# Performance work log

Measured on AMD Instinct MI355X. Metric: run time of the kernel, lower is better.

Reference implementation:

```python
import jax, jax.numpy as jnp
import numpy as np

ROUTINGS = 3
EPS = 1e-05


def squash(x, axis):
    n = jnp.linalg.norm(x, axis=axis, keepdims=True)
    n2 = n * n
    return n2 / (1.0 + n2) * x / (n + EPS)


def setup_inputs() -> dict:
    key = jax.random.key(0)
    k1, k2, k3 = jax.random.split(key, 3)
    B, I, O = 64, 1024, 1024
    stdv = 1.0 / np.sqrt(I)
    u = jax.random.normal(k1, (B, I), dtype=jnp.float32)
    weight = jax.random.uniform(k2, (I, O), dtype=jnp.float32, minval=-stdv, maxval=stdv)
    bias = jax.random.uniform(k3, (O,), dtype=jnp.float32, minval=-stdv, maxval=stdv)
    return {"u": u, "weight": weight, "bias": bias}


def reference(u, weight, bias):
    # u: [B, I], weight: [I, O], bias: [O]
    O = weight.shape[1]
    u_hat = u[:, :, None] * weight  # [B, I, O]
    # retain_grad=False: routing iterations use detached u_hat / bias
    uh = jax.lax.stop_gradient(u_hat)
    bs = jax.lax.stop_gradient(bias)
    c = jnp.full((1, 1, O), 1.0 / O, dtype=u.dtype)  # softmax(zeros) over out dim
    b = jnp.zeros_like(uh)
    for _ in range(ROUTINGS - 1):
        v = squash(jnp.sum(uh * c, axis=1) + bs, axis=1)  # [B, O]
        b = b + uh * v[:, None, :]
        c = jax.nn.softmax(b, axis=2)
    return squash(jnp.sum(u_hat * c, axis=1) + bias, axis=1)
```

## Files before the change

### kernel.cpp

```cpp
#include <hip/hip_runtime.h>
#include <math.h>


#define BB 64
#define II 1024
#define OO 1024
#define EPSF 1e-5f
#define LOG2E 1.44269504088896340736f

__device__ __forceinline__ float wave_sum(float v) {
    #pragma unroll
    for (int off = 32; off > 0; off >>= 1)
        v += __shfl_xor(v, off, 64);
    return v;
}
__device__ __forceinline__ float rfl(float x) {
    return __int_as_float(__builtin_amdgcn_readfirstlane(__float_as_int(x)));
}

template<int IBLKS>
__global__ __launch_bounds__(256)
__attribute__((amdgpu_waves_per_eu(8)))
void stage_k(
    const float* __restrict__ u, const float* __restrict__ w,
    const float* __restrict__ v, float* __restrict__ part)
{
    constexpr int IPB = II / IBLKS;
    constexpr int NG  = IPB / 8;
    static_assert(IPB % 8 == 0, "need groups of 8");
    const int bg   = blockIdx.x / IBLKS;
    const int iblk = blockIdx.x % IBLKS;
    const int wave = threadIdx.x >> 6;
    const int lane = threadIdx.x & 63;
    const int b    = bg * 4 + wave;
    const float4* w4 = (const float4*)w;
    const float4* v4 = (const float4*)(v + b * OO);

    float vv[16];
    #pragma unroll
    for (int j = 0; j < 4; j++) {
        float4 a = v4[j * 64 + lane];
        vv[j*4+0]=a.x*LOG2E; vv[j*4+1]=a.y*LOG2E;
        vv[j*4+2]=a.z*LOG2E; vv[j*4+3]=a.w*LOG2E;
    }
    float ar[16];
    #pragma unroll
    for (int k = 0; k < 16; k++) ar[k] = 0.f;

    const int i0 = iblk * IPB;
    #pragma unroll 1
    for (int g = 0; g < NG; g++) {
        const int ib = i0 + g * 8;

        float us[8];
        #pragma unroll
        for (int ii = 0; ii < 8; ii++)
            us[ii] = rfl(u[b * II + ib + ii]);

        float sA[8];
        #pragma unroll 2
        for (int ii = 0; ii < 8; ii++) {
            const int i = ib + ii;
            float a0;
            {
                float4 t = w4[i * 256 + 0 * 64 + lane];
                a0 = __builtin_amdgcn_exp2f((t.x * vv[0]) * us[ii])
                   + __builtin_amdgcn_exp2f((t.y * vv[1]) * us[ii])
                   + __builtin_amdgcn_exp2f((t.z * vv[2]) * us[ii])
                   + __builtin_amdgcn_exp2f((t.w * vv[3]) * us[ii]);
            }
            #pragma unroll
            for (int j = 1; j < 4; j++) {
                float4 t = w4[i * 256 + j * 64 + lane];
                a0 += __builtin_amdgcn_exp2f((t.x * vv[j*4+0]) * us[ii])
                    + __builtin_amdgcn_exp2f((t.y * vv[j*4+1]) * us[ii])
                    + __builtin_amdgcn_exp2f((t.z * vv[j*4+2]) * us[ii])
                    + __builtin_amdgcn_exp2f((t.w * vv[j*4+3]) * us[ii]);
            }
            sA[ii] = a0;
        }
        #pragma unroll
        for (int off = 32; off > 0; off >>= 1) {
            #pragma unroll
            for (int ii = 0; ii < 8; ii++)
                sA[ii] += __shfl_xor(sA[ii], off, 64);
        }
        float qs[8];
        #pragma unroll
        for (int ii = 0; ii < 8; ii++)
            qs[ii] = rfl(us[ii] * __builtin_amdgcn_rcpf(sA[ii]));

        #pragma unroll 2
        for (int ii = 0; ii < 8; ii++) {
            const int i = ib + ii;
            #pragma unroll
            for (int j = 0; j < 4; j++) {
                float4 t = w4[i * 256 + j * 64 + lane];
                float p;
                p = __builtin_amdgcn_exp2f((t.x * vv[j*4+0]) * us[ii]);
                ar[j*4+0] = fmaf(t.x * p, qs[ii], ar[j*4+0]);
                p = __builtin_amdgcn_exp2f((t.y * vv[j*4+1]) * us[ii]);
                ar[j*4+1] = fmaf(t.y * p, qs[ii], ar[j*4+1]);
                p = __builtin_amdgcn_exp2f((t.z * vv[j*4+2]) * us[ii]);
                ar[j*4+2] = fmaf(t.z * p, qs[ii], ar[j*4+2]);
                p = __builtin_amdgcn_exp2f((t.w * vv[j*4+3]) * us[ii]);
                ar[j*4+3] = fmaf(t.w * p, qs[ii], ar[j*4+3]);
            }
        }
    }
    float4* dst = (float4*)(part + ((size_t)iblk * BB + b) * OO);
    #pragma unroll
    for (int j = 0; j < 4; j++) {
        float4 o;
        o.x = ar[j*4+0]; o.y = ar[j*4+1]; o.z = ar[j*4+2]; o.w = ar[j*4+3];
        dst[j * 64 + lane] = o;
    }
}

template<int IBLKS>
__global__ __launch_bounds__(256)
__attribute__((amdgpu_waves_per_eu(8)))
void gemm_k(
    const float* __restrict__ u, const float* __restrict__ w,
    float* __restrict__ part)
{
    constexpr int IPB = II / IBLKS;
    const int bg   = blockIdx.x / IBLKS;
    const int iblk = blockIdx.x % IBLKS;
    const int wave = threadIdx.x >> 6;
    const int lane = threadIdx.x & 63;
    const int b    = bg * 4 + wave;
    const float4* w4 = (const float4*)w;

    float ar[16];
    #pragma unroll
    for (int k = 0; k < 16; k++) ar[k] = 0.f;

    const int i0 = iblk * IPB;
    #pragma unroll 2
    for (int ii = 0; ii < IPB; ii++) {
        const int i = i0 + ii;
        const float ub = rfl(u[b * II + i]);
        #pragma unroll
        for (int j = 0; j < 4; j++) {
            float4 t = w4[i * 256 + j * 64 + lane];
            ar[j*4+0] = fmaf(ub, t.x, ar[j*4+0]);
            ar[j*4+1] = fmaf(ub, t.y, ar[j*4+1]);
            ar[j*4+2] = fmaf(ub, t.z, ar[j*4+2]);
            ar[j*4+3] = fmaf(ub, t.w, ar[j*4+3]);
        }
    }
    float4* dst = (float4*)(part + ((size_t)iblk * BB + b) * OO);
    #pragma unroll
    for (int j = 0; j < 4; j++) {
        float4 o;
        o.x = ar[j*4+0]; o.y = ar[j*4+1]; o.z = ar[j*4+2]; o.w = ar[j*4+3];
        dst[j * 64 + lane] = o;
    }
}

__global__ __launch_bounds__(1024) void reduce_squash(
    const float* __restrict__ part, const float* __restrict__ bias,
    float* __restrict__ vbuf, float* __restrict__ out,
    float scale, int mode, int nblk)
{
    const int b  = blockIdx.x;
    const int t  = threadIdx.x;
    const int qd = t & 255;
    const int sl = t >> 8;
    const int per = nblk >> 2;
    const float4* p4 = (const float4*)part;

    float4 a0 = make_float4(0.f, 0.f, 0.f, 0.f), a1 = a0;
    const int k0 = sl * per;
    #pragma unroll 2
    for (int k = 0; k < per; k += 2) {
        float4 p0 = p4[(size_t)((k0 + k)     * BB + b) * 256 + qd];
        float4 p1 = p4[(size_t)((k0 + k + 1) * BB + b) * 256 + qd];
        a0.x += p0.x; a0.y += p0.y; a0.z += p0.z; a0.w += p0.w;
        a1.x += p1.x; a1.y += p1.y; a1.z += p1.z; a1.w += p1.w;
    }
    a0.x += a1.x; a0.y += a1.y; a0.z += a1.z; a0.w += a1.w;

    __shared__ float4 redq[1024];
    redq[t] = a0;
    __syncthreads();

    float ss = 0.f;
    float4 x;
    if (t < 256) {
        float4 r0 = redq[qd], r1 = redq[256 + qd],
               r2 = redq[512 + qd], r3 = redq[768 + qd];
        float4 s;
        s.x = (r0.x + r1.x) + (r2.x + r3.x);
        s.y = (r0.y + r1.y) + (r2.y + r3.y);
        s.z = (r0.z + r1.z) + (r2.z + r3.z);
        s.w = (r0.w + r1.w) + (r2.w + r3.w);
        float4 bb = ((const float4*)bias)[qd];
        x.x = fmaf(s.x, scale, bb.x); x.y = fmaf(s.y, scale, bb.y);
        x.z = fmaf(s.z, scale, bb.z); x.w = fmaf(s.w, scale, bb.w);
        ss = x.x*x.x + x.y*x.y + x.z*x.z + x.w*x.w;
    }
    ss = wave_sum(ss);
    __shared__ float red2[16];
    if ((t & 63) == 0) red2[t >> 6] = ss;
    __syncthreads();
    const float tot = (red2[0] + red2[1]) + (red2[2] + red2[3]);

    if (t < 256) {
        const float n = sqrtf(tot);
        const float f = tot / ((1.f + tot) * (n + EPSF));
        float4 vo;
        vo.x = x.x * f; vo.y = x.y * f; vo.z = x.z * f; vo.w = x.w * f;
        if (mode == 0) {
            ((float4*)(vbuf + b * OO))[qd] = vo;
        } else if (mode == 1) {
            float4 pv = ((const float4*)(vbuf + b * OO))[qd];
            pv.x += vo.x; pv.y += vo.y; pv.z += vo.z; pv.w += vo.w;
            ((float4*)(vbuf + b * OO))[qd] = pv;
        } else {
            ((float4*)(out + b * OO))[qd] = vo;
        }
    }
}

template<int IBLKS>
static void run_pipeline(const float* u, const float* w, const float* bias,
                         float* out, void* d_ws, hipStream_t stream)
{
    float* part = (float*)d_ws;
    float* vbuf = part + (size_t)IBLKS * BB * OO;
    dim3 g((BB / 4) * IBLKS), blk(256), rblk(1024);
    gemm_k<IBLKS><<<g, blk, 0, stream>>>(u, w, part);
    reduce_squash<<<dim3(BB), rblk, 0, stream>>>(part, bias, vbuf, out,
                                                 1.0f / (float)OO, 0, IBLKS);
    stage_k<IBLKS><<<g, blk, 0, stream>>>(u, w, vbuf, part);
    reduce_squash<<<dim3(BB), rblk, 0, stream>>>(part, bias, vbuf, out,
                                                 1.0f, 1, IBLKS);
    stage_k<IBLKS><<<g, blk, 0, stream>>>(u, w, vbuf, part);
    reduce_squash<<<dim3(BB), rblk, 0, stream>>>(part, bias, vbuf, out,
                                                 1.0f, 2, IBLKS);
}

extern "C" void kernel_launch(void* const* d_in, const int* in_sizes, int n_in,
                              void* d_out, int out_size, void* d_ws, size_t ws_size,
                              hipStream_t stream) {
    (void)in_sizes; (void)n_in; (void)out_size;
    const float* u    = (const float*)d_in[0];
    const float* w    = (const float*)d_in[1];
    const float* bias = (const float*)d_in[2];
    float* out = (float*)d_out;

    const size_t row = (size_t)BB * OO * sizeof(float);
    if      (ws_size >= 129 * row) run_pipeline<128>(u, w, bias, out, d_ws, stream);
    else if (ws_size >=  65 * row) run_pipeline<64>(u, w, bias, out, d_ws, stream);
    else if (ws_size >=  33 * row) run_pipeline<32>(u, w, bias, out, d_ws, stream);
    else                           run_pipeline<16>(u, w, bias, out, d_ws, stream);
}
```

Measured before the change: 163.0 us.

## Fuse routing pipeline into one persistent kernel with grid-wide barriers

Replaces the six separate launches (gemm, three reduces, two routing stages) with one persistent kernel of 256 blocks of 1024 threads. Spin-wait atomic barriers separate the phases, and a memset resets the counters first. The aim is to remove launch gaps and tail effects between the small kernels. The split changes to 64 I-blocks, and the fallback path uses fixed 8-way splitting. The grid-wide barrier depends on all 256 blocks being co-resident, which could deadlock if they are not, and reductions now run on only 64 of the blocks while the rest sit idle.

```diff
diff --git a/kernel.cpp b/kernel.cpp
--- a/kernel.cpp
+++ b/kernel.cpp
@@ -7,6 +7,9 @@
 #define OO 1024
 #define EPSF 1e-5f
 #define LOG2E 1.44269504088896340736f
+#define NBLK 256
+#define MIBLKS 64
+#define MIPB (II / MIBLKS)
 
 __device__ __forceinline__ float wave_sum(float v) {
     #pragma unroll
@@ -18,21 +21,57 @@
     return __int_as_float(__builtin_amdgcn_readfirstlane(__float_as_int(x)));
 }
 
-template<int IBLKS>
-__global__ __launch_bounds__(256)
-__attribute__((amdgpu_waves_per_eu(8)))
-void stage_k(
-    const float* __restrict__ u, const float* __restrict__ w,
-    const float* __restrict__ v, float* __restrict__ part)
-{
-    constexpr int IPB = II / IBLKS;
-    constexpr int NG  = IPB / 8;
-    static_assert(IPB % 8 == 0, "need groups of 8");
-    const int bg   = blockIdx.x / IBLKS;
-    const int iblk = blockIdx.x % IBLKS;
-    const int wave = threadIdx.x >> 6;
-    const int lane = threadIdx.x & 63;
-    const int b    = bg * 4 + wave;
+__device__ __forceinline__ void gbar(int* c) {
+    __syncthreads();
+    if (threadIdx.x == 0) {
+        __threadfence();
+        __hip_atomic_fetch_add(c, 1, __ATOMIC_RELAXED, __HIP_MEMORY_SCOPE_AGENT);
+        while (__hip_atomic_load(c, __ATOMIC_ACQUIRE,
+                                 __HIP_MEMORY_SCOPE_AGENT) < NBLK) { }
+    }
+    __syncthreads();
+}
+
+
+template<int IPB>
+__device__ __forceinline__ void gemm_wave(
+    const float* __restrict__ u, const float* __restrict__ w,
+    float* __restrict__ part, int b, int iblk, int lane)
+{
+    const float4* w4 = (const float4*)w;
+    float ar[16];
+    #pragma unroll
+    for (int k = 0; k < 16; k++) ar[k] = 0.f;
+    const int i0 = iblk * IPB;
+    #pragma unroll 2
+    for (int ii = 0; ii < IPB; ii++) {
+        const int i = i0 + ii;
+        const float ub = rfl(u[b * II + i]);
+        #pragma unroll
+        for (int j = 0; j < 4; j++) {
+            float4 t = w4[i * 256 + j * 64 + lane];
+            ar[j*4+0] = fmaf(ub, t.x, ar[j*4+0]);
+            ar[j*4+1] = fmaf(ub, t.y, ar[j*4+1]);
+            ar[j*4+2] = fmaf(ub, t.z, ar[j*4+2]);
+            ar[j*4+3] = fmaf(ub, t.w, ar[j*4+3]);
+        }
+    }
+    float4* dst = (float4*)(part + ((size_t)iblk * BB + b) * OO);
+    #pragma unroll
+    for (int j = 0; j < 4; j++) {
+        float4 o;
+        o.x = ar[j*4+0]; o.y = ar[j*4+1]; o.z = ar[j*4+2]; o.w = ar[j*4+3];
+        dst[j * 64 + lane] = o;
+    }
+}
+
+template<int IPB>
+__device__ __forceinline__ void stage_wave(
+    const float* __restrict__ u, const float* __restrict__ w,
+    const float* __restrict__ v, float* __restrict__ part,
+    int b, int iblk, int lane)
+{
+    constexpr int NG = IPB / 8;
     const float4* w4 = (const float4*)w;
     const float4* v4 = (const float4*)(v + b * OO);
 
@@ -51,7 +90,6 @@
     #pragma unroll 1
     for (int g = 0; g < NG; g++) {
         const int ib = i0 + g * 8;
-
         float us[8];
         #pragma unroll
         for (int ii = 0; ii < 8; ii++)
@@ -61,16 +99,9 @@
         #pragma unroll 2
         for (int ii = 0; ii < 8; ii++) {
             const int i = ib + ii;
-            float a0;
-            {
-                float4 t = w4[i * 256 + 0 * 64 + lane];
-                a0 = __builtin_amdgcn_exp2f((t.x * vv[0]) * us[ii])
-                   + __builtin_amdgcn_exp2f((t.y * vv[1]) * us[ii])
-                   + __builtin_amdgcn_exp2f((t.z * vv[2]) * us[ii])
-                   + __builtin_amdgcn_exp2f((t.w * vv[3]) * us[ii]);
-            }
+            float a0 = 0.f;
             #pragma unroll
-            for (int j = 1; j < 4; j++) {
+            for (int j = 0; j < 4; j++) {
                 float4 t = w4[i * 256 + j * 64 + lane];
                 a0 += __builtin_amdgcn_exp2f((t.x * vv[j*4+0]) * us[ii])
                     + __builtin_amdgcn_exp2f((t.y * vv[j*4+1]) * us[ii])
@@ -117,54 +148,11 @@
     }
 }
 
-template<int IBLKS>
-__global__ __launch_bounds__(256)
-__attribute__((amdgpu_waves_per_eu(8)))
-void gemm_k(
-    const float* __restrict__ u, const float* __restrict__ w,
-    float* __restrict__ part)
-{
-    constexpr int IPB = II / IBLKS;
-    const int bg   = blockIdx.x / IBLKS;
-    const int iblk = blockIdx.x % IBLKS;
-    const int wave = threadIdx.x >> 6;
-    const int lane = threadIdx.x & 63;
-    const int b    = bg * 4 + wave;
-    const float4* w4 = (const float4*)w;
-
-    float ar[16];
-    #pragma unroll
-    for (int k = 0; k < 16; k++) ar[k] = 0.f;
-
-    const int i0 = iblk * IPB;
-    #pragma unroll 2
-    for (int ii = 0; ii < IPB; ii++) {
-        const int i = i0 + ii;
-        const float ub = rfl(u[b * II + i]);
-        #pragma unroll
-        for (int j = 0; j < 4; j++) {
-            float4 t = w4[i * 256 + j * 64 + lane];
-            ar[j*4+0] = fmaf(ub, t.x, ar[j*4+0]);
-            ar[j*4+1] = fmaf(ub, t.y, ar[j*4+1]);
-            ar[j*4+2] = fmaf(ub, t.z, ar[j*4+2]);
-            ar[j*4+3] = fmaf(ub, t.w, ar[j*4+3]);
-        }
-    }
-    float4* dst = (float4*)(part + ((size_t)iblk * BB + b) * OO);
-    #pragma unroll
-    for (int j = 0; j < 4; j++) {
-        float4 o;
-        o.x = ar[j*4+0]; o.y = ar[j*4+1]; o.z = ar[j*4+2]; o.w = ar[j*4+3];
-        dst[j * 64 + lane] = o;
-    }
-}
-
-__global__ __launch_bounds__(1024) void reduce_squash(
+__device__ __forceinline__ void reduce_block(
     const float* __restrict__ part, const float* __restrict__ bias,
     float* __restrict__ vbuf, float* __restrict__ out,
-    float scale, int mode, int nblk)
-{
-    const int b  = blockIdx.x;
+    float scale, int mode, int nblk, int b, float4* redq, float* red2)
+{
     const int t  = threadIdx.x;
     const int qd = t & 255;
     const int sl = t >> 8;
@@ -182,7 +170,6 @@
     }
     a0.x += a1.x; a0.y += a1.y; a0.z += a1.z; a0.w += a1.w;
 
-    __shared__ float4 redq[1024];
     redq[t] = a0;
     __syncthreads();
 
@@ -202,7 +189,6 @@
         ss = x.x*x.x + x.y*x.y + x.z*x.z + x.w*x.w;
     }
     ss = wave_sum(ss);
-    __shared__ float red2[16];
     if ((t & 63) == 0) red2[t >> 6] = ss;
     __syncthreads();
     const float tot = (red2[0] + red2[1]) + (red2[2] + red2[3]);
@@ -222,24 +208,69 @@
             ((float4*)(out + b * OO))[qd] = vo;
         }
     }
-}
-
-template<int IBLKS>
-static void run_pipeline(const float* u, const float* w, const float* bias,
-                         float* out, void* d_ws, hipStream_t stream)
-{
-    float* part = (float*)d_ws;
-    float* vbuf = part + (size_t)IBLKS * BB * OO;
-    dim3 g((BB / 4) * IBLKS), blk(256), rblk(1024);
-    gemm_k<IBLKS><<<g, blk, 0, stream>>>(u, w, part);
-    reduce_squash<<<dim3(BB), rblk, 0, stream>>>(part, bias, vbuf, out,
-                                                 1.0f / (float)OO, 0, IBLKS);
-    stage_k<IBLKS><<<g, blk, 0, stream>>>(u, w, vbuf, part);
-    reduce_squash<<<dim3(BB), rblk, 0, stream>>>(part, bias, vbuf, out,
-                                                 1.0f, 1, IBLKS);
-    stage_k<IBLKS><<<g, blk, 0, stream>>>(u, w, vbuf, part);
-    reduce_squash<<<dim3(BB), rblk, 0, stream>>>(part, bias, vbuf, out,
-                                                 1.0f, 2, IBLKS);
+    __syncthreads();
+}
+
+__global__ __launch_bounds__(1024) void capsule_mega(
+    const float* __restrict__ u, const float* __restrict__ w,
+    const float* __restrict__ bias, float* __restrict__ out,
+    float* __restrict__ part, float* __restrict__ vbuf, int* __restrict__ ctr)
+{
+    const int blk  = blockIdx.x;
+    const int wv   = threadIdx.x >> 6;
+    const int lane = threadIdx.x & 63;
+    const int gw   = blk * 16 + wv;
+    const int b_s  = gw & 63;
+    const int ib_s = gw >> 6;
+
+    __shared__ float4 redq[1024];
+    __shared__ float  red2[16];
+
+    gemm_wave<MIPB>(u, w, part, b_s, ib_s, lane);
+    gbar(ctr + 0);
+    if (blk < BB)
+        reduce_block(part, bias, vbuf, out, 1.0f / (float)OO, 0, MIBLKS,
+                     blk, redq, red2);
+    gbar(ctr + 1);
+    stage_wave<MIPB>(u, w, vbuf, part, b_s, ib_s, lane);
+    gbar(ctr + 2);
+    if (blk < BB)
+        reduce_block(part, bias, vbuf, out, 1.0f, 1, MIBLKS, blk, redq, red2);
+    gbar(ctr + 3);
+    stage_wave<MIPB>(u, w, vbuf, part, b_s, ib_s, lane);
+    gbar(ctr + 4);
+    if (blk < BB)
+        reduce_block(part, bias, vbuf, out, 1.0f, 2, MIBLKS, blk, redq, red2);
+}
+
+#define FIBLKS 8
+#define FIPB (II / FIBLKS)
+
+__global__ __launch_bounds__(256) void gemm_fb(
+    const float* __restrict__ u, const float* __restrict__ w,
+    float* __restrict__ part)
+{
+    const int bg = blockIdx.x / FIBLKS, iblk = blockIdx.x % FIBLKS;
+    const int wave = threadIdx.x >> 6, lane = threadIdx.x & 63;
+    gemm_wave<FIPB>(u, w, part, bg * 4 + wave, iblk, lane);
+}
+__global__ __launch_bounds__(256) void stage_fb(
+    const float* __restrict__ u, const float* __restrict__ w,
+    const float* __restrict__ v, float* __restrict__ part)
+{
+    const int bg = blockIdx.x / FIBLKS, iblk = blockIdx.x % FIBLKS;
+    const int wave = threadIdx.x >> 6, lane = threadIdx.x & 63;
+    stage_wave<FIPB>(u, w, v, part, bg * 4 + wave, iblk, lane);
+}
+__global__ __launch_bounds__(1024) void reduce_fb(
+    const float* __restrict__ part, const float* __restrict__ bias,
+    float* __restrict__ vbuf, float* __restrict__ out,
+    float scale, int mode, int nblk)
+{
+    __shared__ float4 redq[1024];
+    __shared__ float  red2[16];
+    reduce_block(part, bias, vbuf, out, scale, mode, nblk,
+                 blockIdx.x, redq, red2);
 }
 
 extern "C" void kernel_launch(void* const* d_in, const int* in_sizes, int n_in,
@@ -251,9 +282,27 @@
     const float* bias = (const float*)d_in[2];
     float* out = (float*)d_out;
 
-    const size_t row = (size_t)BB * OO * sizeof(float);
-    if      (ws_size >= 129 * row) run_pipeline<128>(u, w, bias, out, d_ws, stream);
-    else if (ws_size >=  65 * row) run_pipeline<64>(u, w, bias, out, d_ws, stream);
-    else if (ws_size >=  33 * row) run_pipeline<32>(u, w, bias, out, d_ws, stream);
-    else                           run_pipeline<16>(u, w, bias, out, d_ws, stream);
-}
+    const size_t row = (size_t)BB * OO;
+    const size_t mega_need = (MIBLKS + 1) * row * 4 + 256;
+    if (ws_size >= mega_need) {
+        float* part = (float*)d_ws;
+        float* vbuf = part + MIBLKS * row;
+        int*   ctr  = (int*)(vbuf + row);
+        hipMemsetAsync(ctr, 0, 8 * sizeof(int), stream);
+        capsule_mega<<<dim3(NBLK), dim3(1024), 0, stream>>>(
+            u, w, bias, out, part, vbuf, ctr);
+    } else {
+        float* part = (float*)d_ws;
+        float* vbuf = part + FIBLKS * row;
+        dim3 g((BB / 4) * FIBLKS), blk(256), rblk(1024);
+        gemm_fb<<<g, blk, 0, stream>>>(u, w, part);
+        reduce_fb<<<dim3(BB), rblk, 0, stream>>>(part, bias, vbuf, out,
+                                                 1.0f / (float)OO, 0, FIBLKS);
+        stage_fb<<<g, blk, 0, stream>>>(u, w, vbuf, part);
+        reduce_fb<<<dim3(BB), rblk, 0, stream>>>(part, bias, vbuf, out,
+                                                 1.0f, 1, FIBLKS);
+        stage_fb<<<g, blk, 0, stream>>>(u, w, vbuf, part);
+        reduce_fb<<<dim3(BB), rblk, 0, stream>>>(part, bias, vbuf, out,
+                                                 1.0f, 2, FIBLKS);
+    }
+}
```

After: 281.7 us. 72.9% more time.
